# Performance work log

Measured on AMD Instinct MI355X. Metric: run time of the kernel, lower is better.

Reference implementation:

```python
import jax, jax.numpy as jnp
import numpy as np

N_NODES = 100000
N_EDGES = 1600000
IN_FEATS = 64
HIDDEN = 64
NUM_CLASSES = 2


def setup_inputs() -> dict:
    key = jax.random.key(0)
    ks = jax.random.split(key, 9)
    feat = jax.random.normal(ks[0], (N_NODES, IN_FEATS), dtype=jnp.float32)
    src = jax.random.randint(ks[1], (N_EDGES,), 0, N_NODES, dtype=jnp.int64) if jax.config.jax_enable_x64 else jax.random.randint(ks[1], (N_EDGES,), 0, N_NODES).astype(jnp.int32)
    dst = jax.random.randint(ks[2], (N_EDGES,), 0, N_NODES).astype(src.dtype)
    s_in = 1.0 / np.sqrt(IN_FEATS)
    s_e = 1.0 / np.sqrt(2 * HIDDEN)
    s_o = 1.0 / np.sqrt(HIDDEN)
    W_in = jax.random.uniform(ks[3], (IN_FEATS, HIDDEN), jnp.float32, -s_in, s_in)
    b_in = jax.random.uniform(ks[4], (HIDDEN,), jnp.float32, -s_in, s_in)
    W_edge = jax.random.uniform(ks[5], (2 * HIDDEN, 1), jnp.float32, -s_e, s_e)
    b_edge = jax.random.uniform(ks[6], (1,), jnp.float32, -s_e, s_e)
    W_out = jax.random.uniform(ks[7], (HIDDEN, NUM_CLASSES), jnp.float32, -s_o, s_o)
    b_out = jax.random.uniform(ks[8], (NUM_CLASSES,), jnp.float32, -s_o, s_o)
    return {"feat": feat, "src": src, "dst": dst, "W_in": W_in, "b_in": b_in,
            "W_edge": W_edge, "b_edge": b_edge, "W_out": W_out, "b_out": b_out}


def reference(feat, src, dst, W_in, b_in, W_edge, b_edge, W_out, b_out):
    # input node MLP: [N, in] @ [in, H]
    h = feat @ W_in + b_in  # [N, H]
    # edge function: sigmoid(Linear(cat(h_src, h_dst))) -- split concat to avoid [E, 2H] buffer
    hu = h[src]  # [E, H]
    hv = h[dst]  # [E, H]
    W_u, W_v = W_edge[:HIDDEN], W_edge[HIDDEN:]  # each [H, 1]
    w = jax.nn.sigmoid(hu @ W_u + hv @ W_v + b_edge)  # [E, 1]
    # message = h_src * w, reduce = sum over incoming edges at dst
    msgs = hu * w  # [E, H]
    agg = jax.ops.segment_sum(msgs, dst, num_segments=N_NODES)  # [N, H]
    # DGL UDF-reduce semantics: zero in-degree nodes keep previous h
    deg = jax.ops.segment_sum(jnp.ones((dst.shape[0],), dtype=jnp.float32), dst, num_segments=N_NODES)
    h_new = jnp.where(deg[:, None] > 0, agg, h)
    return h_new @ W_out + b_out  # [N, num_classes]
```

## Files before the change

kernel.cpp:

```cpp
#include <hip/hip_runtime.h>
#include <math.h>

#define N_NODES 100000
#define N_EDGES 1600000

#define BK_LOG 7
#define BKW 128
#define NBK ((N_NODES + BKW - 1) / BKW)
#define CAPB 2688
#define UNS4 3

#define GS 400
#define EPS (N_EDGES / GS)
#define EPS4 (EPS / 4)

#define NT_BLOCKS ((N_NODES + 63) / 64)

__global__ __launch_bounds__(256) void prep_kernel(
    const float* __restrict__ feat,
    const float* __restrict__ W_in,
    const float* __restrict__ b_in,
    const float* __restrict__ W_edge,
    const float* __restrict__ W_out,
    const int*   __restrict__ src,
    const int*   __restrict__ dst,
    int* __restrict__ cursor,
    int* __restrict__ ework,
    float4* __restrict__ nodeT)
{
    const int tid = threadIdx.x;

    if ((int)blockIdx.x < GS) {
        __shared__ int hist[NBK];
        __shared__ int base[NBK];
        for (int i = tid; i < NBK; i += 256) hist[i] = 0;
        __syncthreads();

        const int4* src4 = (const int4*)src;
        const int4* dst4 = (const int4*)dst;
        const int   b40  = (int)blockIdx.x * EPS4;

        int bb[16], rr[16], pk[16];
        #pragma unroll
        for (int j = 0; j < 4; ++j) {
            const int o4 = j * 256 + tid;
            if (o4 < EPS4) {
                const int4 d4 = dst4[b40 + o4];
                const int4 s4 = src4[b40 + o4];
                const int dv[4] = {d4.x, d4.y, d4.z, d4.w};
                const int sv[4] = {s4.x, s4.y, s4.z, s4.w};
                #pragma unroll
                for (int u = 0; u < 4; ++u) {
                    const int idx = j * 4 + u;
                    const int d = dv[u];
                    const int b = d >> BK_LOG;
                    bb[idx] = b;
                    rr[idx] = atomicAdd(&hist[b], 1);
                    pk[idx] = ((d & (BKW - 1)) << 17) | sv[u];
                }
            }
        }
        __syncthreads();

        for (int b = tid; b < NBK; b += 256) {
            const int c = hist[b];
            if (c) base[b] = atomicAdd(&cursor[b], c);
        }
        __syncthreads();

        #pragma unroll
        for (int j = 0; j < 4; ++j) {
            const int o4 = j * 256 + tid;
            if (o4 < EPS4) {
                #pragma unroll
                for (int u = 0; u < 4; ++u) {
                    const int idx = j * 4 + u;
                    ework[bb[idx] * CAPB + base[bb[idx]] + rr[idx]] = pk[idx];
                }
            }
        }
        return;
    }

    __shared__ float sP[64 * 4];
    __shared__ float sQ[64 * 4];
    __shared__ float sc[4];

    if (tid < 64) {
        sP[tid * 4 + 0] = W_edge[tid];
        sP[tid * 4 + 1] = W_out[tid * 2 + 0];
        sP[tid * 4 + 2] = W_out[tid * 2 + 1];
        sP[tid * 4 + 3] = W_edge[64 + tid];
    }
    __syncthreads();

    {
        const int k = tid >> 2, j = tid & 3;
        float q = 0.f;
        for (int m = 0; m < 64; ++m) q += W_in[k * 64 + m] * sP[m * 4 + j];
        sQ[k * 4 + j] = q;
        if (tid < 4) {
            float cc = 0.f;
            for (int m = 0; m < 64; ++m) cc += b_in[m] * sP[m * 4 + tid];
            sc[tid] = cc;
        }
    }
    __syncthreads();

    const int lane = tid & 63;
    const int wv   = tid >> 6;
    const int n    = ((int)blockIdx.x - GS) * 64 + wv * 16 + (lane >> 2);
    const int ks   = (lane & 3) << 4;

    float p0 = 0.f, p1 = 0.f, p2 = 0.f, p3 = 0.f;
    if (n < N_NODES) {
        const float* fr = feat + (size_t)n * 64 + ks;
        #pragma unroll
        for (int i4 = 0; i4 < 4; ++i4) {
            const float4 f = *(const float4*)(fr + i4 * 4);
            const float fv[4] = {f.x, f.y, f.z, f.w};
            #pragma unroll
            for (int u = 0; u < 4; ++u) {
                const float4 q = *(const float4*)&sQ[(ks + i4 * 4 + u) * 4];
                p0 += fv[u] * q.x;
                p1 += fv[u] * q.y;
                p2 += fv[u] * q.z;
                p3 += fv[u] * q.w;
            }
        }
    }
    #pragma unroll
    for (int off = 1; off <= 2; off <<= 1) {
        p0 += __shfl_xor(p0, off);
        p1 += __shfl_xor(p1, off);
        p2 += __shfl_xor(p2, off);
        p3 += __shfl_xor(p3, off);
    }
    if (n < N_NODES && (lane & 3) == 0)
        nodeT[n] = make_float4(p0 + sc[0], p1 + sc[1], p2 + sc[2], p3 + sc[3]);
}

__global__ __launch_bounds__(256) void sortagg_kernel(
    const int* __restrict__ ework,
    const int* __restrict__ cursor,
    const float4* __restrict__ nodeT,
    const float* __restrict__ b_edge,
    const float* __restrict__ b_out,
    float2* __restrict__ out)
{
    __shared__ int hist[BKW];
    __shared__ int sbase[BKW];
    __shared__ int wtot[2];
    __shared__ int ssorted[CAPB];

    const int b   = blockIdx.x;
    const int tid = threadIdx.x;

    if (tid < BKW) hist[tid] = 0;
    __syncthreads();

    const int cnt = min(cursor[b], CAPB);
    const int4* ew4 = (const int4*)(ework + b * CAPB);

    int4 vv[UNS4];
    int  rk[UNS4][4];
    #pragma unroll
    for (int j = 0; j < UNS4; ++j) {
        const int o = (j * 256 + tid) * 4;
        if (o < cnt) {
            const int4 v = ew4[j * 256 + tid];
            vv[j] = v;
            const int ve[4] = {v.x, v.y, v.z, v.w};
            #pragma unroll
            for (int u = 0; u < 4; ++u)
                if (o + u < cnt) rk[j][u] = atomicAdd(&hist[ve[u] >> 17], 1);
        }
    }
    __syncthreads();

    int own = 0, inc = 0;
    if (tid < BKW) { own = hist[tid]; inc = own; }
    #pragma unroll
    for (int off = 1; off < 64; off <<= 1) {
        const int t = __shfl_up(inc, off);
        if ((tid & 63) >= off) inc += t;
    }
    if (tid < BKW && (tid & 63) == 63) wtot[tid >> 6] = inc;
    __syncthreads();
    if (tid < BKW) sbase[tid] = inc - own + ((tid >= 64) ? wtot[0] : 0);
    __syncthreads();

    #pragma unroll
    for (int j = 0; j < UNS4; ++j) {
        const int o = (j * 256 + tid) * 4;
        if (o < cnt) {
            const int4 v = vv[j];
            const int ve[4] = {v.x, v.y, v.z, v.w};
            #pragma unroll
            for (int u = 0; u < 4; ++u)
                if (o + u < cnt)
                    ssorted[sbase[ve[u] >> 17] + rk[j][u]] = ve[u] & 0x1FFFF;
        }
    }
    __syncthreads();

    const int sub = tid & 3;
    const float be  = b_edge[0];
    const float bo0 = b_out[0];
    const float bo1 = b_out[1];

    #pragma unroll
    for (int pass = 0; pass < 2; ++pass) {
        const int l = pass * 64 + (tid >> 2);
        const int n = b * BKW + l;

        float4 tn = make_float4(0.f, 0.f, 0.f, 0.f);
        if (n < N_NODES) tn = nodeT[n];
        const int   beg = sbase[l];
        const int   len = hist[l];
        const float Bn  = tn.w + be;

        float m0 = 0.f, m1 = 0.f;
        int i = sub;
        for (; i + 4 < len; i += 8) {
            const int s0 = ssorted[beg + i];
            const int s1 = ssorted[beg + i + 4];
            const float4 t0 = nodeT[s0];
            const float4 t1 = nodeT[s1];
            const float w0 = 1.0f / (1.0f + __expf(-(t0.x + Bn)));
            const float w1 = 1.0f / (1.0f + __expf(-(t1.x + Bn)));
            m0 += w0 * t0.y + w1 * t1.y;
            m1 += w0 * t0.z + w1 * t1.z;
        }
        if (i < len) {
            const int s0 = ssorted[beg + i];
            const float4 t0 = nodeT[s0];
            const float w0 = 1.0f / (1.0f + __expf(-(t0.x + Bn)));
            m0 += w0 * t0.y;
            m1 += w0 * t0.z;
        }
        m0 += __shfl_xor(m0, 1);
        m1 += __shfl_xor(m1, 1);
        m0 += __shfl_xor(m0, 2);
        m1 += __shfl_xor(m1, 2);

        if (sub == 0 && n < N_NODES) {
            const float o0 = (len ? m0 : tn.y) + bo0;
            const float o1 = (len ? m1 : tn.z) + bo1;
            out[n] = make_float2(o0, o1);
        }
    }
}

extern "C" void kernel_launch(void* const* d_in, const int* in_sizes, int n_in,
                              void* d_out, int out_size, void* d_ws, size_t ws_size,
                              hipStream_t stream) {
    const float* feat   = (const float*)d_in[0];
    const int*   src    = (const int*)d_in[1];
    const int*   dst    = (const int*)d_in[2];
    const float* W_in   = (const float*)d_in[3];
    const float* b_in   = (const float*)d_in[4];
    const float* W_edge = (const float*)d_in[5];
    const float* b_edge = (const float*)d_in[6];
    const float* W_out  = (const float*)d_in[7];
    const float* b_out  = (const float*)d_in[8];
    float2* out = (float2*)d_out;

    float4* nodeT  = (float4*)d_ws;
    int*    ework  = (int*)(nodeT + N_NODES);
    int*    cursor = ework + NBK * CAPB;

    hipMemsetAsync(cursor, 0, NBK * sizeof(int), stream);

    prep_kernel<<<GS + NT_BLOCKS, 256, 0, stream>>>(
        feat, W_in, b_in, W_edge, W_out, src, dst, cursor, ework, nodeT);
    sortagg_kernel<<<NBK, 256, 0, stream>>>(
        ework, cursor, nodeT, b_edge, b_out, out);
}
```

Before: 127.1 us.

## Replace per-bucket LDS sort with shared-memory float atomics aggregation

The aggregation kernel no longer counting-sorts edges within each 128-node bucket. Instead it gathers nodeT per edge and accumulates the weighted messages directly into shared-memory float atomics, and it caches the destination node terms in LDS. The scatter phase now makes two passes over dst (a histogram pass, then a pass that places edges with per-bucket LDS atomics), so fewer scatter blocks are needed (GS lowered to 128) and register arrays go away. The cost is extra dst reads, contended LDS float atomics, and float summation order that is no longer deterministic.

Result: slower. 137.6 us (+8.2%).

```diff
diff --git a/kernel.cpp b/kernel.cpp
--- a/kernel.cpp
+++ b/kernel.cpp
@@ -10,9 +10,10 @@
 #define CAPB 2688
 #define UNS4 3
 
-#define GS 400
+#define GS 128
 #define EPS (N_EDGES / GS)
 #define EPS4 (EPS / 4)
+#define SROUNDS ((EPS4 + 255) / 256)
 
 #define NT_BLOCKS ((N_NODES + 63) / 64)
 
@@ -32,17 +33,34 @@
 
     if ((int)blockIdx.x < GS) {
         __shared__ int hist[NBK];
-        __shared__ int base[NBK];
-        for (int i = tid; i < NBK; i += 256) hist[i] = 0;
+        __shared__ int rhist[NBK];
+        __shared__ int gbase[NBK];
+        for (int i = tid; i < NBK; i += 256) { hist[i] = 0; rhist[i] = 0; }
         __syncthreads();
 
         const int4* src4 = (const int4*)src;
         const int4* dst4 = (const int4*)dst;
         const int   b40  = (int)blockIdx.x * EPS4;
 
-        int bb[16], rr[16], pk[16];
-        #pragma unroll
-        for (int j = 0; j < 4; ++j) {
+        for (int j = 0; j < SROUNDS; ++j) {
+            const int o4 = j * 256 + tid;
+            if (o4 < EPS4) {
+                const int4 d4 = dst4[b40 + o4];
+                atomicAdd(&hist[d4.x >> BK_LOG], 1);
+                atomicAdd(&hist[d4.y >> BK_LOG], 1);
+                atomicAdd(&hist[d4.z >> BK_LOG], 1);
+                atomicAdd(&hist[d4.w >> BK_LOG], 1);
+            }
+        }
+        __syncthreads();
+
+        for (int i = tid; i < NBK; i += 256) {
+            const int c = hist[i];
+            if (c) gbase[i] = atomicAdd(&cursor[i], c);
+        }
+        __syncthreads();
+
+        for (int j = 0; j < SROUNDS; ++j) {
             const int o4 = j * 256 + tid;
             if (o4 < EPS4) {
                 const int4 d4 = dst4[b40 + o4];
@@ -51,31 +69,11 @@
                 const int sv[4] = {s4.x, s4.y, s4.z, s4.w};
                 #pragma unroll
                 for (int u = 0; u < 4; ++u) {
-                    const int idx = j * 4 + u;
                     const int d = dv[u];
                     const int b = d >> BK_LOG;
-                    bb[idx] = b;
-                    rr[idx] = atomicAdd(&hist[b], 1);
-                    pk[idx] = ((d & (BKW - 1)) << 17) | sv[u];
-                }
-            }
-        }
-        __syncthreads();
-
-        for (int b = tid; b < NBK; b += 256) {
-            const int c = hist[b];
-            if (c) base[b] = atomicAdd(&cursor[b], c);
-        }
-        __syncthreads();
-
-        #pragma unroll
-        for (int j = 0; j < 4; ++j) {
-            const int o4 = j * 256 + tid;
-            if (o4 < EPS4) {
-                #pragma unroll
-                for (int u = 0; u < 4; ++u) {
-                    const int idx = j * 4 + u;
-                    ework[bb[idx] * CAPB + base[bb[idx]] + rr[idx]] = pk[idx];
+                    const int r = atomicAdd(&rhist[b], 1);
+                    ework[b * CAPB + gbase[b] + r] =
+                        ((d & (BKW - 1)) << 17) | sv[u];
                 }
             }
         }
@@ -140,7 +138,7 @@
         nodeT[n] = make_float4(p0 + sc[0], p1 + sc[1], p2 + sc[2], p3 + sc[3]);
 }
 
-__global__ __launch_bounds__(256) void sortagg_kernel(
+__global__ __launch_bounds__(256) void agg_kernel(
     const int* __restrict__ ework,
     const int* __restrict__ cursor,
     const float4* __restrict__ nodeT,
@@ -148,106 +146,57 @@
     const float* __restrict__ b_out,
     float2* __restrict__ out)
 {
-    __shared__ int hist[BKW];
-    __shared__ int sbase[BKW];
-    __shared__ int wtot[2];
-    __shared__ int ssorted[CAPB];
+    __shared__ float4 sT[BKW];
+    __shared__ float  aM0[BKW];
+    __shared__ float  aM1[BKW];
+    __shared__ int    aC[BKW];
 
     const int b   = blockIdx.x;
     const int tid = threadIdx.x;
 
-    if (tid < BKW) hist[tid] = 0;
+    if (tid < BKW) {
+        const int n = b * BKW + tid;
+        float4 t = make_float4(0.f, 0.f, 0.f, 0.f);
+        if (n < N_NODES) t = nodeT[n];
+        t.w += b_edge[0];
+        sT[tid] = t;
+        aM0[tid] = 0.f;
+        aM1[tid] = 0.f;
+        aC[tid]  = 0;
+    }
     __syncthreads();
 
     const int cnt = min(cursor[b], CAPB);
     const int4* ew4 = (const int4*)(ework + b * CAPB);
 
-    int4 vv[UNS4];
-    int  rk[UNS4][4];
     #pragma unroll
     for (int j = 0; j < UNS4; ++j) {
         const int o = (j * 256 + tid) * 4;
         if (o < cnt) {
             const int4 v = ew4[j * 256 + tid];
-            vv[j] = v;
             const int ve[4] = {v.x, v.y, v.z, v.w};
             #pragma unroll
-            for (int u = 0; u < 4; ++u)
-                if (o + u < cnt) rk[j][u] = atomicAdd(&hist[ve[u] >> 17], 1);
-        }
-    }
-    __syncthreads();
-
-    int own = 0, inc = 0;
-    if (tid < BKW) { own = hist[tid]; inc = own; }
-    #pragma unroll
-    for (int off = 1; off < 64; off <<= 1) {
-        const int t = __shfl_up(inc, off);
-        if ((tid & 63) >= off) inc += t;
-    }
-    if (tid < BKW && (tid & 63) == 63) wtot[tid >> 6] = inc;
-    __syncthreads();
-    if (tid < BKW) sbase[tid] = inc - own + ((tid >= 64) ? wtot[0] : 0);
-    __syncthreads();
-
-    #pragma unroll
-    for (int j = 0; j < UNS4; ++j) {
-        const int o = (j * 256 + tid) * 4;
-        if (o < cnt) {
-            const int4 v = vv[j];
-            const int ve[4] = {v.x, v.y, v.z, v.w};
-            #pragma unroll
-            for (int u = 0; u < 4; ++u)
-                if (o + u < cnt)
-                    ssorted[sbase[ve[u] >> 17] + rk[j][u]] = ve[u] & 0x1FFFF;
-        }
-    }
-    __syncthreads();
-
-    const int sub = tid & 3;
-    const float be  = b_edge[0];
-    const float bo0 = b_out[0];
-    const float bo1 = b_out[1];
-
-    #pragma unroll
-    for (int pass = 0; pass < 2; ++pass) {
-        const int l = pass * 64 + (tid >> 2);
-        const int n = b * BKW + l;
-
-        float4 tn = make_float4(0.f, 0.f, 0.f, 0.f);
-        if (n < N_NODES) tn = nodeT[n];
-        const int   beg = sbase[l];
-        const int   len = hist[l];
-        const float Bn  = tn.w + be;
-
-        float m0 = 0.f, m1 = 0.f;
-        int i = sub;
-        for (; i + 4 < len; i += 8) {
-            const int s0 = ssorted[beg + i];
-            const int s1 = ssorted[beg + i + 4];
-            const float4 t0 = nodeT[s0];
-            const float4 t1 = nodeT[s1];
-            const float w0 = 1.0f / (1.0f + __expf(-(t0.x + Bn)));
-            const float w1 = 1.0f / (1.0f + __expf(-(t1.x + Bn)));
-            m0 += w0 * t0.y + w1 * t1.y;
-            m1 += w0 * t0.z + w1 * t1.z;
-        }
-        if (i < len) {
-            const int s0 = ssorted[beg + i];
-            const float4 t0 = nodeT[s0];
-            const float w0 = 1.0f / (1.0f + __expf(-(t0.x + Bn)));
-            m0 += w0 * t0.y;
-            m1 += w0 * t0.z;
-        }
-        m0 += __shfl_xor(m0, 1);
-        m1 += __shfl_xor(m1, 1);
-        m0 += __shfl_xor(m0, 2);
-        m1 += __shfl_xor(m1, 2);
-
-        if (sub == 0 && n < N_NODES) {
-            const float o0 = (len ? m0 : tn.y) + bo0;
-            const float o1 = (len ? m1 : tn.z) + bo1;
-            out[n] = make_float2(o0, o1);
+            for (int u = 0; u < 4; ++u) {
+                if (o + u < cnt) {
+                    const int    l = ve[u] >> 17;
+                    const int    s = ve[u] & 0x1FFFF;
+                    const float4 t = nodeT[s];
+                    const float  w = 1.0f / (1.0f + __expf(-(t.x + sT[l].w)));
+                    atomicAdd(&aM0[l], w * t.y);
+                    atomicAdd(&aM1[l], w * t.z);
+                    atomicAdd(&aC[l], 1);
+                }
+            }
+        }
+    }
+    __syncthreads();
+
+    if (tid < BKW) {
+        const int n = b * BKW + tid;
+        if (n < N_NODES) {
+            const bool has = aC[tid] > 0;
+            out[n] = make_float2((has ? aM0[tid] : sT[tid].y) + b_out[0],
+                                 (has ? aM1[tid] : sT[tid].z) + b_out[1]);
         }
     }
 }
@@ -274,6 +223,6 @@
 
     prep_kernel<<<GS + NT_BLOCKS, 256, 0, stream>>>(
         feat, W_in, b_in, W_edge, W_out, src, dst, cursor, ework, nodeT);
-    sortagg_kernel<<<NBK, 256, 0, stream>>>(
+    agg_kernel<<<NBK, 256, 0, stream>>>(
         ework, cursor, nodeT, b_edge, b_out, out);
 }
```

## Fuse memset, prep and sort-aggregate into one cooperative persistent kernel

Applied to the files above, without the earlier changes.

Replaces the memset plus two kernel launches with a single cooperative kernel that uses grid-wide syncs between phases. The phases are cursor zeroing, edge bucketing with node projection, and per-bucket sort and aggregation, and blocks loop over work chunks persistently. The aim is to remove launch overhead and the gaps between kernels. In exchange it adds grid-sync cost, caps the grid at 1024 blocks, and raises shared memory per block, which may limit occupancy and per-phase parallelism.

Measured after the change: 236.8 us. +86.2%, slower.

```diff
diff --git a/kernel.cpp b/kernel.cpp
--- a/kernel.cpp
+++ b/kernel.cpp
@@ -1,5 +1,8 @@
 #include <hip/hip_runtime.h>
+#include <hip/hip_cooperative_groups.h>
 #include <math.h>
+
+namespace cg = cooperative_groups;
 
 #define N_NODES 100000
 #define N_EDGES 1600000
@@ -15,76 +18,40 @@
 #define EPS4 (EPS / 4)
 
 #define NT_BLOCKS ((N_NODES + 63) / 64)
-
-__global__ __launch_bounds__(256) void prep_kernel(
+#define NCHUNK (GS + NT_BLOCKS)
+#define MAXGRID 1024
+
+__global__ __launch_bounds__(256, 4) void fused_kernel(
     const float* __restrict__ feat,
     const float* __restrict__ W_in,
     const float* __restrict__ b_in,
     const float* __restrict__ W_edge,
+    const float* __restrict__ b_edge,
     const float* __restrict__ W_out,
+    const float* __restrict__ b_out,
     const int*   __restrict__ src,
     const int*   __restrict__ dst,
     int* __restrict__ cursor,
     int* __restrict__ ework,
-    float4* __restrict__ nodeT)
+    float4* __restrict__ nodeT,
+    float2* __restrict__ out)
 {
+    cg::grid_group gg = cg::this_grid();
     const int tid = threadIdx.x;
-
-    if ((int)blockIdx.x < GS) {
-        __shared__ int hist[NBK];
-        __shared__ int base[NBK];
-        for (int i = tid; i < NBK; i += 256) hist[i] = 0;
-        __syncthreads();
-
-        const int4* src4 = (const int4*)src;
-        const int4* dst4 = (const int4*)dst;
-        const int   b40  = (int)blockIdx.x * EPS4;
-
-        int bb[16], rr[16], pk[16];
-        #pragma unroll
-        for (int j = 0; j < 4; ++j) {
-            const int o4 = j * 256 + tid;
-            if (o4 < EPS4) {
-                const int4 d4 = dst4[b40 + o4];
-                const int4 s4 = src4[b40 + o4];
-                const int dv[4] = {d4.x, d4.y, d4.z, d4.w};
-                const int sv[4] = {s4.x, s4.y, s4.z, s4.w};
-                #pragma unroll
-                for (int u = 0; u < 4; ++u) {
-                    const int idx = j * 4 + u;
-                    const int d = dv[u];
-                    const int b = d >> BK_LOG;
-                    bb[idx] = b;
-                    rr[idx] = atomicAdd(&hist[b], 1);
-                    pk[idx] = ((d & (BKW - 1)) << 17) | sv[u];
-                }
-            }
-        }
-        __syncthreads();
-
-        for (int b = tid; b < NBK; b += 256) {
-            const int c = hist[b];
-            if (c) base[b] = atomicAdd(&cursor[b], c);
-        }
-        __syncthreads();
-
-        #pragma unroll
-        for (int j = 0; j < 4; ++j) {
-            const int o4 = j * 256 + tid;
-            if (o4 < EPS4) {
-                #pragma unroll
-                for (int u = 0; u < 4; ++u) {
-                    const int idx = j * 4 + u;
-                    ework[bb[idx] * CAPB + base[bb[idx]] + rr[idx]] = pk[idx];
-                }
-            }
-        }
-        return;
-    }
+    const int bid = blockIdx.x;
+    const int nb  = gridDim.x;
 
     __shared__ float sP[64 * 4];
     __shared__ float sQ[64 * 4];
     __shared__ float sc[4];
+    __shared__ int   hist[NBK];
+    __shared__ int   base[NBK];
+    __shared__ int   ahist[BKW];
+    __shared__ int   abase[BKW];
+    __shared__ int   wtot[2];
+    __shared__ int   ssorted[CAPB];
+
+    for (int i = bid * 256 + tid; i < NBK; i += nb * 256) cursor[i] = 0;
 
     if (tid < 64) {
         sP[tid * 4 + 0] = W_edge[tid];
@@ -93,7 +60,6 @@
         sP[tid * 4 + 3] = W_edge[64 + tid];
     }
     __syncthreads();
-
     {
         const int k = tid >> 2, j = tid & 3;
         float q = 0.f;
@@ -107,147 +73,190 @@
     }
     __syncthreads();
 
-    const int lane = tid & 63;
-    const int wv   = tid >> 6;
-    const int n    = ((int)blockIdx.x - GS) * 64 + wv * 16 + (lane >> 2);
-    const int ks   = (lane & 3) << 4;
-
-    float p0 = 0.f, p1 = 0.f, p2 = 0.f, p3 = 0.f;
-    if (n < N_NODES) {
-        const float* fr = feat + (size_t)n * 64 + ks;
+    gg.sync();
+
+    for (int chunk = bid; chunk < NCHUNK; chunk += nb) {
+        if (chunk < GS) {
+            __syncthreads();
+            for (int i = tid; i < NBK; i += 256) hist[i] = 0;
+            __syncthreads();
+
+            const int4* src4 = (const int4*)src;
+            const int4* dst4 = (const int4*)dst;
+            const int   b40  = chunk * EPS4;
+
+            int bb[16], rr[16], pk[16];
+            #pragma unroll
+            for (int j = 0; j < 4; ++j) {
+                const int o4 = j * 256 + tid;
+                if (o4 < EPS4) {
+                    const int4 d4 = dst4[b40 + o4];
+                    const int4 s4 = src4[b40 + o4];
+                    const int dv[4] = {d4.x, d4.y, d4.z, d4.w};
+                    const int sv[4] = {s4.x, s4.y, s4.z, s4.w};
+                    #pragma unroll
+                    for (int u = 0; u < 4; ++u) {
+                        const int idx = j * 4 + u;
+                        const int d = dv[u];
+                        const int b = d >> BK_LOG;
+                        bb[idx] = b;
+                        rr[idx] = atomicAdd(&hist[b], 1);
+                        pk[idx] = ((d & (BKW - 1)) << 17) | sv[u];
+                    }
+                }
+            }
+            __syncthreads();
+
+            for (int b = tid; b < NBK; b += 256) {
+                const int c = hist[b];
+                if (c) base[b] = atomicAdd(&cursor[b], c);
+            }
+            __syncthreads();
+
+            #pragma unroll
+            for (int j = 0; j < 4; ++j) {
+                const int o4 = j * 256 + tid;
+                if (o4 < EPS4) {
+                    #pragma unroll
+                    for (int u = 0; u < 4; ++u) {
+                        const int idx = j * 4 + u;
+                        ework[bb[idx] * CAPB + base[bb[idx]] + rr[idx]] = pk[idx];
+                    }
+                }
+            }
+        } else {
+            const int c    = chunk - GS;
+            const int lane = tid & 63;
+            const int wv   = tid >> 6;
+            const int n    = c * 64 + wv * 16 + (lane >> 2);
+            const int ks   = (lane & 3) << 4;
+
+            float p0 = 0.f, p1 = 0.f, p2 = 0.f, p3 = 0.f;
+            if (n < N_NODES) {
+                const float* fr = feat + (size_t)n * 64 + ks;
+                #pragma unroll
+                for (int i4 = 0; i4 < 4; ++i4) {
+                    const float4 f = *(const float4*)(fr + i4 * 4);
+                    const float fv[4] = {f.x, f.y, f.z, f.w};
+                    #pragma unroll
+                    for (int u = 0; u < 4; ++u) {
+                        const float4 q = *(const float4*)&sQ[(ks + i4 * 4 + u) * 4];
+                        p0 += fv[u] * q.x;
+                        p1 += fv[u] * q.y;
+                        p2 += fv[u] * q.z;
+                        p3 += fv[u] * q.w;
+                    }
+                }
+            }
+            #pragma unroll
+            for (int off = 1; off <= 2; off <<= 1) {
+                p0 += __shfl_xor(p0, off);
+                p1 += __shfl_xor(p1, off);
+                p2 += __shfl_xor(p2, off);
+                p3 += __shfl_xor(p3, off);
+            }
+            if (n < N_NODES && (lane & 3) == 0)
+                nodeT[n] = make_float4(p0 + sc[0], p1 + sc[1], p2 + sc[2], p3 + sc[3]);
+        }
+    }
+
+    gg.sync();
+
+    for (int b = bid; b < NBK; b += nb) {
+        __syncthreads();
+        if (tid < BKW) ahist[tid] = 0;
+        __syncthreads();
+
+        const int cnt = min(cursor[b], CAPB);
+        const int4* ew4 = (const int4*)(ework + b * CAPB);
+
+        int4 vv[UNS4];
+        int  rk[UNS4][4];
         #pragma unroll
-        for (int i4 = 0; i4 < 4; ++i4) {
-            const float4 f = *(const float4*)(fr + i4 * 4);
-            const float fv[4] = {f.x, f.y, f.z, f.w};
-            #pragma unroll
-            for (int u = 0; u < 4; ++u) {
-                const float4 q = *(const float4*)&sQ[(ks + i4 * 4 + u) * 4];
-                p0 += fv[u] * q.x;
-                p1 += fv[u] * q.y;
-                p2 += fv[u] * q.z;
-                p3 += fv[u] * q.w;
-            }
-        }
-    }
-    #pragma unroll
-    for (int off = 1; off <= 2; off <<= 1) {
-        p0 += __shfl_xor(p0, off);
-        p1 += __shfl_xor(p1, off);
-        p2 += __shfl_xor(p2, off);
-        p3 += __shfl_xor(p3, off);
-    }
-    if (n < N_NODES && (lane & 3) == 0)
-        nodeT[n] = make_float4(p0 + sc[0], p1 + sc[1], p2 + sc[2], p3 + sc[3]);
-}
-
-__global__ __launch_bounds__(256) void sortagg_kernel(
-    const int* __restrict__ ework,
-    const int* __restrict__ cursor,
-    const float4* __restrict__ nodeT,
-    const float* __restrict__ b_edge,
-    const float* __restrict__ b_out,
-    float2* __restrict__ out)
-{
-    __shared__ int hist[BKW];
-    __shared__ int sbase[BKW];
-    __shared__ int wtot[2];
-    __shared__ int ssorted[CAPB];
-
-    const int b   = blockIdx.x;
-    const int tid = threadIdx.x;
-
-    if (tid < BKW) hist[tid] = 0;
-    __syncthreads();
-
-    const int cnt = min(cursor[b], CAPB);
-    const int4* ew4 = (const int4*)(ework + b * CAPB);
-
-    int4 vv[UNS4];
-    int  rk[UNS4][4];
-    #pragma unroll
-    for (int j = 0; j < UNS4; ++j) {
-        const int o = (j * 256 + tid) * 4;
-        if (o < cnt) {
-            const int4 v = ew4[j * 256 + tid];
-            vv[j] = v;
-            const int ve[4] = {v.x, v.y, v.z, v.w};
-            #pragma unroll
-            for (int u = 0; u < 4; ++u)
-                if (o + u < cnt) rk[j][u] = atomicAdd(&hist[ve[u] >> 17], 1);
-        }
-    }
-    __syncthreads();
-
-    int own = 0, inc = 0;
-    if (tid < BKW) { own = hist[tid]; inc = own; }
-    #pragma unroll
-    for (int off = 1; off < 64; off <<= 1) {
-        const int t = __shfl_up(inc, off);
-        if ((tid & 63) >= off) inc += t;
-    }
-    if (tid < BKW && (tid & 63) == 63) wtot[tid >> 6] = inc;
-    __syncthreads();
-    if (tid < BKW) sbase[tid] = inc - own + ((tid >= 64) ? wtot[0] : 0);
-    __syncthreads();
-
-    #pragma unroll
-    for (int j = 0; j < UNS4; ++j) {
-        const int o = (j * 256 + tid) * 4;
-        if (o < cnt) {
-            const int4 v = vv[j];
-            const int ve[4] = {v.x, v.y, v.z, v.w};
-            #pragma unroll
-            for (int u = 0; u < 4; ++u)
-                if (o + u < cnt)
-                    ssorted[sbase[ve[u] >> 17] + rk[j][u]] = ve[u] & 0x1FFFF;
-        }
-    }
-    __syncthreads();
-
-    const int sub = tid & 3;
-    const float be  = b_edge[0];
-    const float bo0 = b_out[0];
-    const float bo1 = b_out[1];
-
-    #pragma unroll
-    for (int pass = 0; pass < 2; ++pass) {
-        const int l = pass * 64 + (tid >> 2);
-        const int n = b * BKW + l;
-
-        float4 tn = make_float4(0.f, 0.f, 0.f, 0.f);
-        if (n < N_NODES) tn = nodeT[n];
-        const int   beg = sbase[l];
-        const int   len = hist[l];
-        const float Bn  = tn.w + be;
-
-        float m0 = 0.f, m1 = 0.f;
-        int i = sub;
-        for (; i + 4 < len; i += 8) {
-            const int s0 = ssorted[beg + i];
-            const int s1 = ssorted[beg + i + 4];
-            const float4 t0 = nodeT[s0];
-            const float4 t1 = nodeT[s1];
-            const float w0 = 1.0f / (1.0f + __expf(-(t0.x + Bn)));
-            const float w1 = 1.0f / (1.0f + __expf(-(t1.x + Bn)));
-            m0 += w0 * t0.y + w1 * t1.y;
-            m1 += w0 * t0.z + w1 * t1.z;
-        }
-        if (i < len) {
-            const int s0 = ssorted[beg + i];
-            const float4 t0 = nodeT[s0];
-            const float w0 = 1.0f / (1.0f + __expf(-(t0.x + Bn)));
-            m0 += w0 * t0.y;
-            m1 += w0 * t0.z;
-        }
-        m0 += __shfl_xor(m0, 1);
-        m1 += __shfl_xor(m1, 1);
-        m0 += __shfl_xor(m0, 2);
-        m1 += __shfl_xor(m1, 2);
-
-        if (sub == 0 && n < N_NODES) {
-            const float o0 = (len ? m0 : tn.y) + bo0;
-            const float o1 = (len ? m1 : tn.z) + bo1;
-            out[n] = make_float2(o0, o1);
+        for (int j = 0; j < UNS4; ++j) {
+            const int o = (j * 256 + tid) * 4;
+            if (o < cnt) {
+                const int4 v = ew4[j * 256 + tid];
+                vv[j] = v;
+                const int ve[4] = {v.x, v.y, v.z, v.w};
+                #pragma unroll
+                for (int u = 0; u < 4; ++u)
+                    if (o + u < cnt) rk[j][u] = atomicAdd(&ahist[ve[u] >> 17], 1);
+            }
+        }
+        __syncthreads();
+
+        int own = 0, inc = 0;
+        if (tid < BKW) { own = ahist[tid]; inc = own; }
+        #pragma unroll
+        for (int off = 1; off < 64; off <<= 1) {
+            const int t = __shfl_up(inc, off);
+            if ((tid & 63) >= off) inc += t;
+        }
+        if (tid < BKW && (tid & 63) == 63) wtot[tid >> 6] = inc;
+        __syncthreads();
+        if (tid < BKW) abase[tid] = inc - own + ((tid >= 64) ? wtot[0] : 0);
+        __syncthreads();
+
+        #pragma unroll
+        for (int j = 0; j < UNS4; ++j) {
+            const int o = (j * 256 + tid) * 4;
+            if (o < cnt) {
+                const int4 v = vv[j];
+                const int ve[4] = {v.x, v.y, v.z, v.w};
+                #pragma unroll
+                for (int u = 0; u < 4; ++u)
+                    if (o + u < cnt)
+                        ssorted[abase[ve[u] >> 17] + rk[j][u]] = ve[u] & 0x1FFFF;
+            }
+        }
+        __syncthreads();
+
+        const int sub = tid & 3;
+        const float be  = b_edge[0];
+        const float bo0 = b_out[0];
+        const float bo1 = b_out[1];
+
+        #pragma unroll
+        for (int pass = 0; pass < 2; ++pass) {
+            const int l = pass * 64 + (tid >> 2);
+            const int n = b * BKW + l;
+
+            float4 tn = make_float4(0.f, 0.f, 0.f, 0.f);
+            if (n < N_NODES) tn = nodeT[n];
+            const int   beg = abase[l];
+            const int   len = ahist[l];
+            const float Bn  = tn.w + be;
+
+            float m0 = 0.f, m1 = 0.f;
+            int i = sub;
+            for (; i + 4 < len; i += 8) {
+                const int s0 = ssorted[beg + i];
+                const int s1 = ssorted[beg + i + 4];
+                const float4 t0 = nodeT[s0];
+                const float4 t1 = nodeT[s1];
+                const float w0 = 1.0f / (1.0f + __expf(-(t0.x + Bn)));
+                const float w1 = 1.0f / (1.0f + __expf(-(t1.x + Bn)));
+                m0 += w0 * t0.y + w1 * t1.y;
+                m1 += w0 * t0.z + w1 * t1.z;
+            }
+            if (i < len) {
+                const int s0 = ssorted[beg + i];
+                const float4 t0 = nodeT[s0];
+                const float w0 = 1.0f / (1.0f + __expf(-(t0.x + Bn)));
+                m0 += w0 * t0.y;
+                m1 += w0 * t0.z;
+            }
+            m0 += __shfl_xor(m0, 1);
+            m1 += __shfl_xor(m1, 1);
+            m0 += __shfl_xor(m0, 2);
+            m1 += __shfl_xor(m1, 2);
+
+            if (sub == 0 && n < N_NODES) {
+                const float o0 = (len ? m0 : tn.y) + bo0;
+                const float o1 = (len ? m1 : tn.z) + bo1;
+                out[n] = make_float2(o0, o1);
+            }
         }
     }
 }
@@ -270,10 +279,24 @@
     int*    ework  = (int*)(nodeT + N_NODES);
     int*    cursor = ework + NBK * CAPB;
 
-    hipMemsetAsync(cursor, 0, NBK * sizeof(int), stream);
-
-    prep_kernel<<<GS + NT_BLOCKS, 256, 0, stream>>>(
-        feat, W_in, b_in, W_edge, W_out, src, dst, cursor, ework, nodeT);
-    sortagg_kernel<<<NBK, 256, 0, stream>>>(
-        ework, cursor, nodeT, b_edge, b_out, out);
+    static int grid = 0;
+    if (grid == 0) {
+        int maxB = 0;
+        if (hipOccupancyMaxActiveBlocksPerMultiprocessor(
+                &maxB, fused_kernel, 256, 0) != hipSuccess || maxB < 1)
+            maxB = 4;
+        long g = (long)maxB * 256;
+        if (g > MAXGRID) g = MAXGRID;
+        if (g < 256) g = 256;
+        grid = (int)g;
+    }
+
+    void* args[] = {
+        (void*)&feat, (void*)&W_in, (void*)&b_in, (void*)&W_edge,
+        (void*)&b_edge, (void*)&W_out, (void*)&b_out, (void*)&src,
+        (void*)&dst, (void*)&cursor, (void*)&ework, (void*)&nodeT,
+        (void*)&out
+    };
+    hipLaunchCooperativeKernel((void*)fused_kernel, dim3(grid), dim3(256),
+                               args, 0, stream);
 }
```

## Use fewer edge-scatter blocks with two-pass histogram then scatter

Applied to the files above, without the earlier changes.

Cuts the number of scatter blocks from 400 to 128, so each block handles about three times as many edges. The single register-buffered pass becomes a histogram pass over dst followed by a second pass that rereads dst and src and takes ranks from a separate LDS counter. This means fewer global cursor atomics and no per-edge register arrays. In exchange, dst is read twice and fewer blocks are available for parallelism.

New measurement: 124.4 us. -2.2%, faster.

```diff
diff --git a/kernel.cpp b/kernel.cpp
--- a/kernel.cpp
+++ b/kernel.cpp
@@ -10,9 +10,10 @@
 #define CAPB 2688
 #define UNS4 3
 
-#define GS 400
+#define GS 128
 #define EPS (N_EDGES / GS)
 #define EPS4 (EPS / 4)
+#define SROUNDS ((EPS4 + 255) / 256)
 
 #define NT_BLOCKS ((N_NODES + 63) / 64)
 
@@ -32,17 +33,34 @@
 
     if ((int)blockIdx.x < GS) {
         __shared__ int hist[NBK];
-        __shared__ int base[NBK];
-        for (int i = tid; i < NBK; i += 256) hist[i] = 0;
+        __shared__ int rhist[NBK];
+        __shared__ int gbase[NBK];
+        for (int i = tid; i < NBK; i += 256) { hist[i] = 0; rhist[i] = 0; }
         __syncthreads();
 
         const int4* src4 = (const int4*)src;
         const int4* dst4 = (const int4*)dst;
         const int   b40  = (int)blockIdx.x * EPS4;
 
-        int bb[16], rr[16], pk[16];
-        #pragma unroll
-        for (int j = 0; j < 4; ++j) {
+        for (int j = 0; j < SROUNDS; ++j) {
+            const int o4 = j * 256 + tid;
+            if (o4 < EPS4) {
+                const int4 d4 = dst4[b40 + o4];
+                atomicAdd(&hist[d4.x >> BK_LOG], 1);
+                atomicAdd(&hist[d4.y >> BK_LOG], 1);
+                atomicAdd(&hist[d4.z >> BK_LOG], 1);
+                atomicAdd(&hist[d4.w >> BK_LOG], 1);
+            }
+        }
+        __syncthreads();
+
+        for (int i = tid; i < NBK; i += 256) {
+            const int c = hist[i];
+            if (c) gbase[i] = atomicAdd(&cursor[i], c);
+        }
+        __syncthreads();
+
+        for (int j = 0; j < SROUNDS; ++j) {
             const int o4 = j * 256 + tid;
             if (o4 < EPS4) {
                 const int4 d4 = dst4[b40 + o4];
@@ -51,31 +69,11 @@
                 const int sv[4] = {s4.x, s4.y, s4.z, s4.w};
                 #pragma unroll
                 for (int u = 0; u < 4; ++u) {
-                    const int idx = j * 4 + u;
                     const int d = dv[u];
                     const int b = d >> BK_LOG;
-                    bb[idx] = b;
-                    rr[idx] = atomicAdd(&hist[b], 1);
-                    pk[idx] = ((d & (BKW - 1)) << 17) | sv[u];
-                }
-            }
-        }
-        __syncthreads();
-
-        for (int b = tid; b < NBK; b += 256) {
-            const int c = hist[b];
-            if (c) base[b] = atomicAdd(&cursor[b], c);
-        }
-        __syncthreads();
-
-        #pragma unroll
-        for (int j = 0; j < 4; ++j) {
-            const int o4 = j * 256 + tid;
-            if (o4 < EPS4) {
-                #pragma unroll
-                for (int u = 0; u < 4; ++u) {
-                    const int idx = j * 4 + u;
-                    ework[bb[idx] * CAPB + base[bb[idx]] + rr[idx]] = pk[idx];
+                    const int r = atomicAdd(&rhist[b], 1);
+                    ework[b * CAPB + gbase[b] + r] =
+                        ((d & (BKW - 1)) << 17) | sv[u];
                 }
             }
         }
```
